# Kernel optimization log

Hardware: AMD Instinct MI355X
Metric: run time of the kernel (lower is better)

Reference implementation:

```python
import jax, jax.numpy as jnp
import numpy as np

HIDDEN = 1024
NUM_HEADS = 16
HEAD_DIM = HIDDEN // NUM_HEADS
MASK_BIAS = -10000.0


def setup_inputs() -> dict:
    key = jax.random.key(0)
    ks = jax.random.split(key, 5)
    B, S = 4, 2048
    hidden_states = jax.random.normal(ks[0], (B, S, HIDDEN), dtype=jnp.float32)
    # fused QKV projection (Linear1D_Col): hidden -> 3*hidden
    w_qkv = jax.random.normal(ks[1], (HIDDEN, 3 * HIDDEN), dtype=jnp.float32) * (HIDDEN ** -0.5)
    b_qkv = jax.random.normal(ks[2], (3 * HIDDEN,), dtype=jnp.float32) * 0.02
    # output dense (Linear1D_Row): hidden -> hidden
    w_dense = jax.random.normal(ks[3], (HIDDEN, HIDDEN), dtype=jnp.float32) * (HIDDEN ** -0.5)
    b_dense = jax.random.normal(ks[4], (HIDDEN,), dtype=jnp.float32) * 0.02
    return {"hidden_states": hidden_states, "w_qkv": w_qkv, "b_qkv": b_qkv,
            "w_dense": w_dense, "b_dense": b_dense}


def _split_heads(t):
    # [B, S, H*D] -> [B, H, S, D]
    B, S, _ = t.shape
    return t.reshape(B, S, NUM_HEADS, HEAD_DIM).transpose(0, 2, 1, 3)


def reference(hidden_states, w_qkv, b_qkv, w_dense, b_dense):
    B, S, _ = hidden_states.shape
    kvq = hidden_states @ w_qkv + b_qkv  # [B, S, 3*hidden]
    # NOTE: original chunk order is k, v, q (key first!)
    k, v, q = jnp.split(kvq, 3, axis=-1)
    q = _split_heads(q) * (HEAD_DIM ** -0.5)  # [B, H, S, D]
    k = _split_heads(k)
    v = _split_heads(v)
    scores = jnp.einsum('bhqd,bhkd->bhqk', q, k)  # [B, H, S, S]
    causal = jnp.tril(jnp.ones((S, S), dtype=bool))
    scores = jnp.where(causal[None, None], scores, jnp.asarray(MASK_BIAS, scores.dtype))
    dt = scores.dtype
    attn = jax.nn.softmax(scores.astype(jnp.float32), axis=-1).astype(dt)
    ctx = jnp.einsum('bhqk,bhkd->bhqd', attn, v)  # [B, H, S, D]
    ctx = ctx.transpose(0, 2, 1, 3).reshape(B, S, HIDDEN)
    return ctx @ w_dense + b_dense
```

## Files before the change

### kernel.cpp

```cpp
#include <hip/hip_runtime.h>

#define H_NUM 16
#define HD    64
#define SQ    2048
#define HID   1024
#define MTOK  8192

typedef __attribute__((ext_vector_type(8))) short bf16x8;
typedef __attribute__((ext_vector_type(4))) short s16x4;
typedef __attribute__((ext_vector_type(4))) float f32x4;

__device__ __forceinline__ short f2bf(float f) {
  union { float f; unsigned u; } v; v.f = f;
  unsigned r = v.u + 0x7fffu + ((v.u >> 16) & 1u);
  return (short)(r >> 16);
}

__device__ __forceinline__ float fexp2(float x) {
#if __has_builtin(__builtin_amdgcn_exp2f)
  return __builtin_amdgcn_exp2f(x);
#else
  return exp2f(x);
#endif
}

__device__ __forceinline__ void gload_lds16(const short* g, short* l) {
  __builtin_amdgcn_global_load_lds(
      (const __attribute__((address_space(1))) void*)g,
      (__attribute__((address_space(3))) void*)l, 16, 0, 0);
}

__global__ void k_cvt(const float* __restrict__ in, short* __restrict__ out, int n4) {
  int i = blockIdx.x * blockDim.x + threadIdx.x;
  if (i < n4) {
    float4 f = ((const float4*)in)[i];
    s16x4 o = { f2bf(f.x), f2bf(f.y), f2bf(f.z), f2bf(f.w) };
    ((s16x4*)out)[i] = o;
  }
}

__global__ void k_tr(const float* __restrict__ in, short* __restrict__ out, int R, int C) {
  __shared__ float t[32][33];
  int c0 = blockIdx.x * 32, r0 = blockIdx.y * 32;
  int tx = threadIdx.x, ty = threadIdx.y;
#pragma unroll
  for (int i = 0; i < 4; i++)
    t[ty + 8 * i][tx] = in[(size_t)(r0 + ty + 8 * i) * C + c0 + tx];
  __syncthreads();
#pragma unroll
  for (int i = 0; i < 4; i++)
    out[(size_t)(c0 + ty + 8 * i) * R + r0 + tx] = f2bf(t[tx][ty + 8 * i]);
}

template <int EPI>
__global__ __launch_bounds__(512, 2) void k_gemm(
    const short* __restrict__ A, const short* __restrict__ Bt,
    const float* __restrict__ bias,
    short* __restrict__ qbuf, short* __restrict__ kbuf, short* __restrict__ vtbuf,
    float* __restrict__ outf, int Kd) {
  __shared__ short as[2][16384];
  __shared__ short bs[2][8192];
  const int tid = threadIdx.x;
  const int w = tid >> 6, l = tid & 63;
  const int lr = l & 15, lk = l >> 4;
  const int wm = w >> 1, wn = w & 1;
  const int nwg = gridDim.x * gridDim.y;
  const int lin = blockIdx.y * gridDim.x + blockIdx.x;
  const int swz = (lin & 7) * (nwg >> 3) + (lin >> 3);
  const int m0 = (swz / gridDim.x) * 256, n0 = (swz % gridDim.x) * 128;

  const int NT = Kd >> 6;

#define STAGE_TILE(kt_, bufn_)                                            \
  do {                                                                    \
    _Pragma("unroll")                                                     \
    for (int rnd = 0; rnd < 4; ++rnd) {                                   \
      int g = rnd * 512 + tid;                                            \
      int row = g >> 3;                                                   \
      int sc_ = ((g & 7) * 8) ^ ((row & 7) * 8);                          \
      gload_lds16(A + (size_t)(m0 + row) * Kd + (kt_) + sc_,              \
                  &as[bufn_][0] + g * 8);                                 \
    }                                                                     \
    _Pragma("unroll")                                                     \
    for (int rnd = 0; rnd < 2; ++rnd) {                                   \
      int g = rnd * 512 + tid;                                            \
      int row = g >> 3;                                                   \
      int sc_ = ((g & 7) * 8) ^ ((row & 7) * 8);                          \
      gload_lds16(Bt + (size_t)(n0 + row) * Kd + (kt_) + sc_,             \
                  &bs[bufn_][0] + g * 8);                                 \
    }                                                                     \
  } while (0)

  f32x4 acc[4][4] = {};

  STAGE_TILE(0, 0);

  int buf = 0;
  for (int t = 0; t < NT; ++t) {
    if (t + 1 < NT) {
      STAGE_TILE((t + 1) * 64, buf ^ 1);
      asm volatile("s_waitcnt vmcnt(6)" ::: "memory");
    } else {
      asm volatile("s_waitcnt vmcnt(0)" ::: "memory");
    }
    __builtin_amdgcn_s_barrier();
    __builtin_amdgcn_sched_barrier(0);

    const short* ab = &as[buf][0];
    const short* bb = &bs[buf][0];
    const int cswz = (lr & 7) * 8;
    bf16x8 af[2][4], bfr[2][2];
#pragma unroll
    for (int kk = 0; kk < 2; ++kk)
#pragma unroll
      for (int m = 0; m < 4; ++m) {
        int row = wm * 64 + m * 16 + lr;
        af[kk][m] = *(const bf16x8*)(ab + row * 64 + ((kk * 32 + lk * 8) ^ cswz));
      }
#pragma unroll
    for (int ph = 0; ph < 2; ++ph) {
#pragma unroll
      for (int kk = 0; kk < 2; ++kk)
#pragma unroll
        for (int n = 0; n < 2; ++n) {
          int row = wn * 64 + (ph * 2 + n) * 16 + lr;
          bfr[kk][n] = *(const bf16x8*)(bb + row * 64 + ((kk * 32 + lk * 8) ^ cswz));
        }
      __builtin_amdgcn_s_setprio(1);
#pragma unroll
      for (int kk = 0; kk < 2; ++kk)
#pragma unroll
        for (int m = 0; m < 4; ++m)
#pragma unroll
          for (int n = 0; n < 2; ++n)
            acc[m][ph * 2 + n] = __builtin_amdgcn_mfma_f32_16x16x32_bf16(
                af[kk][m], bfr[kk][n], acc[m][ph * 2 + n], 0, 0, 0);
      __builtin_amdgcn_s_setprio(0);
    }
    __builtin_amdgcn_sched_barrier(0);
    __builtin_amdgcn_s_barrier();
    buf ^= 1;
  }
#undef STAGE_TILE

  const float SCLQ = 0.125f * 1.44269504088896341f;
#pragma unroll
  for (int n = 0; n < 4; ++n) {
    const int col = n0 + wn * 64 + n * 16 + lr;
    const float bv = bias[col];
    if (EPI == 1) {
#pragma unroll
      for (int m = 0; m < 4; ++m) {
        int row = m0 + wm * 64 + m * 16 + lk * 4;
#pragma unroll
        for (int r = 0; r < 4; ++r)
          outf[(size_t)(row + r) * HID + col] = acc[m][n][r] + bv;
      }
    } else if (col < HID) {
      int h = col >> 6, d = col & 63;
#pragma unroll
      for (int m = 0; m < 4; ++m) {
        int row = m0 + wm * 64 + m * 16 + lk * 4;
        int b = row >> 11, s = row & 2047;
#pragma unroll
        for (int r = 0; r < 4; ++r)
          kbuf[((size_t)(b * H_NUM + h) * SQ + s + r) * HD + d] = f2bf(acc[m][n][r] + bv);
      }
    } else if (col < 2 * HID) {
      int f = col - HID, h = f >> 6, d = f & 63;
#pragma unroll
      for (int m = 0; m < 4; ++m) {
        int row = m0 + wm * 64 + m * 16 + lk * 4;
        int b = row >> 11, s = row & 2047;
        s16x4 pk;
#pragma unroll
        for (int r = 0; r < 4; ++r) pk[r] = f2bf(acc[m][n][r] + bv);
        *(s16x4*)&vtbuf[((size_t)(b * H_NUM + h) * HD + d) * SQ + s] = pk;
      }
    } else {
      int f = col - 2 * HID, h = f >> 6, d = f & 63;
#pragma unroll
      for (int m = 0; m < 4; ++m) {
        int row = m0 + wm * 64 + m * 16 + lk * 4;
        int b = row >> 11, s = row & 2047;
#pragma unroll
        for (int r = 0; r < 4; ++r)
          qbuf[((size_t)(b * H_NUM + h) * SQ + s + r) * HD + d] = f2bf((acc[m][n][r] + bv) * SCLQ);
      }
    }
  }
}

__global__ __launch_bounds__(512) void k_attn(
    const short* __restrict__ Q, const short* __restrict__ K,
    const short* __restrict__ Vt, short* __restrict__ ctx) {
  __shared__ short ks[2][4096];
  __shared__ short vs[2][4096];
  __shared__ short ps[8][16][72];
  const int tid = threadIdx.x;
  const int w = tid >> 6, l = tid & 63;
  const int lr = l & 15, lk = l >> 4;
  const int bh = blockIdx.y;
  const int bb = bh >> 4, hh = bh & 15;
  const size_t base = (size_t)bh * (SQ * HD);
  const float THR = 11.5416f;

  const int srow = tid >> 3;
  const int scol = ((tid & 7) * 8) ^ ((srow & 7) * 8);
  const short* kg0 = K + base + srow * HD + scol;
  const short* vg0 = Vt + base + (size_t)srow * SQ + scol;
  short* kld = &ks[0][0] + tid * 8;
  short* vld = &vs[0][0] + tid * 8;
  const int rdswz = (lr & 7) * 8;

  int buf = 0;
  for (int pass = 0; pass < 2; ++pass) {
    const int qt = pass ? (15 - blockIdx.x) : blockIdx.x;
    const int nt = 2 * qt + 2;
    const int diag = 2 * qt + (w >> 2);
    const int qr = qt * 128 + w * 16;

    bf16x8 qf[2];
#pragma unroll
    for (int kk = 0; kk < 2; ++kk)
      qf[kk] = *(const bf16x8*)(Q + base + (size_t)(qr + lr) * HD + kk * 32 + lk * 8);

    f32x4 o[4] = {};
    float mrun = -3.0e4f, lsum = 0.f;

    gload_lds16(kg0, kld + buf * 4096);
    gload_lds16(vg0, vld + buf * 4096);
    __syncthreads();

    for (int t = 0; t < nt; ++t) {
      if (t + 1 < nt) {
        gload_lds16(kg0 + (t + 1) * 4096, kld + (buf ^ 1) * 4096);
        gload_lds16(vg0 + (t + 1) * 64, vld + (buf ^ 1) * 4096);
      }
      if (t <= diag) {
        const short* kb = &ks[buf][0];
        const short* vb = &vs[buf][0];
        f32x4 sf[4] = {};
        __builtin_amdgcn_s_setprio(1);
#pragma unroll
        for (int kk = 0; kk < 2; ++kk)
#pragma unroll
          for (int n = 0; n < 4; ++n) {
            bf16x8 kf = *(const bf16x8*)(kb + (n * 16 + lr) * 64 + ((kk * 32 + lk * 8) ^ rdswz));
            sf[n] = __builtin_amdgcn_mfma_f32_16x16x32_bf16(kf, qf[kk], sf[n], 0, 0, 0);
          }
        __builtin_amdgcn_s_setprio(0);

        if (t == diag) {
          const int qg = qr + lr;
#pragma unroll
          for (int n = 0; n < 4; ++n) {
            int kg = t * 64 + n * 16 + lk * 4;
#pragma unroll
            for (int r = 0; r < 4; ++r)
              if (kg + r > qg) sf[n][r] = -14426.95f;
          }
        }

        float m0 = sf[0][0];
#pragma unroll
        for (int n = 0; n < 4; ++n)
#pragma unroll
          for (int r = 0; r < 4; ++r) m0 = fmaxf(m0, sf[n][r]);
        m0 = fmaxf(m0, __shfl_xor(m0, 16));
        m0 = fmaxf(m0, __shfl_xor(m0, 32));

        if (__any(m0 > mrun + THR)) {
          float mn = fmaxf(mrun, m0);
          float sc = fexp2(mrun - mn);
          float scq[4];
#pragma unroll
          for (int r = 0; r < 4; ++r) scq[r] = __shfl(sc, lk * 4 + r);
#pragma unroll
          for (int nd = 0; nd < 4; ++nd)
#pragma unroll
            for (int r = 0; r < 4; ++r) o[nd][r] *= scq[r];
          lsum *= sc;
          mrun = mn;
        }

        float rs = 0.f;
#pragma unroll
        for (int n = 0; n < 4; ++n) {
          s16x4 pk;
#pragma unroll
          for (int r = 0; r < 4; ++r) {
            float p = fexp2(sf[n][r] - mrun);
            rs += p;
            pk[r] = (short)(__float_as_uint(p) >> 16);
          }
          *(s16x4*)&ps[w][lr][n * 16 + lk * 4] = pk;
        }
        lsum += rs;

        bf16x8 pa[2];
#pragma unroll
        for (int kk = 0; kk < 2; ++kk)
          pa[kk] = *(const bf16x8*)&ps[w][lr][kk * 32 + lk * 8];

        __builtin_amdgcn_s_setprio(1);
#pragma unroll
        for (int kk = 0; kk < 2; ++kk)
#pragma unroll
          for (int nd = 0; nd < 4; ++nd) {
            bf16x8 vf = *(const bf16x8*)(vb + (nd * 16 + lr) * 64 + ((kk * 32 + lk * 8) ^ rdswz));
            o[nd] = __builtin_amdgcn_mfma_f32_16x16x32_bf16(pa[kk], vf, o[nd], 0, 0, 0);
          }
        __builtin_amdgcn_s_setprio(0);
      }
      __syncthreads();
      buf ^= 1;
    }

    lsum += __shfl_xor(lsum, 16);
    lsum += __shfl_xor(lsum, 32);
    float inv = 1.0f / lsum;
    float invq[4];
#pragma unroll
    for (int r = 0; r < 4; ++r) invq[r] = __shfl(inv, lk * 4 + r);
#pragma unroll
    for (int nd = 0; nd < 4; ++nd)
#pragma unroll
      for (int r = 0; r < 4; ++r) {
        int s = qr + lk * 4 + r;
        ctx[((size_t)(bb * SQ + s)) * HID + hh * 64 + nd * 16 + lr] = f2bf(o[nd][r] * invq[r]);
      }
  }
}

extern "C" void kernel_launch(void* const* d_in, const int* in_sizes, int n_in,
                              void* d_out, int out_size, void* d_ws, size_t ws_size,
                              hipStream_t stream) {
  const float* hs   = (const float*)d_in[0];
  const float* wqkv = (const float*)d_in[1];
  const float* bqkv = (const float*)d_in[2];
  const float* wd   = (const float*)d_in[3];
  const float* bd   = (const float*)d_in[4];
  float* out = (float*)d_out;
  char* ws = (char*)d_ws;
  const size_t MB = 1u << 20;

  short* hs_bf  = (short*)(ws);
  short* wqkv_t = (short*)(ws + 16 * MB);
  short* wd_t   = (short*)(ws + 22 * MB);
  short* qbuf   = (short*)(ws + 24 * MB);
  short* kbuf   = (short*)(ws + 40 * MB);
  short* vtbuf  = (short*)(ws + 56 * MB);
  short* ctx    = (short*)(ws + 72 * MB);

  k_cvt<<<8192, 256, 0, stream>>>(hs, hs_bf, MTOK * HID / 4);
  k_tr<<<dim3(96, 32), dim3(32, 8), 0, stream>>>(wqkv, wqkv_t, 1024, 3072);
  k_tr<<<dim3(32, 32), dim3(32, 8), 0, stream>>>(wd, wd_t, 1024, 1024);
  k_gemm<0><<<dim3(24, 32), 512, 0, stream>>>(hs_bf, wqkv_t, bqkv,
                                              qbuf, kbuf, vtbuf, nullptr, 1024);
  k_attn<<<dim3(8, 64), 512, 0, stream>>>(qbuf, kbuf, vtbuf, ctx);
  k_gemm<1><<<dim3(8, 32), 512, 0, stream>>>(ctx, wd_t, bd,
                                             nullptr, nullptr, nullptr, out, 1024);
}
```

Before: 177.4 us.

## Triple-buffer GEMM LDS tiles and interleave global loads with MFMA phases

Moves the projection GEMM from double to triple LDS buffering, prefetching two K-tiles ahead. The global-to-LDS loads are split across four sub-phases of each K-step and interleaved with LDS fragment reads and MFMA groups, separated by barriers. The aim is to hide global memory latency and spread issue pressure. In exchange LDS use rises from 96KB to 144KB per block, which may break the two-blocks-per-CU launch bound, and the extra barriers per iteration add synchronisation overhead.

```diff
diff --git a/kernel.cpp b/kernel.cpp
--- a/kernel.cpp
+++ b/kernel.cpp
@@ -58,8 +58,8 @@
     const float* __restrict__ bias,
     short* __restrict__ qbuf, short* __restrict__ kbuf, short* __restrict__ vtbuf,
     float* __restrict__ outf, int Kd) {
-  __shared__ short as[2][16384];
-  __shared__ short bs[2][8192];
+  __shared__ short as[3][16384];
+  __shared__ short bs[3][8192];
   const int tid = threadIdx.x;
   const int w = tid >> 6, l = tid & 63;
   const int lr = l & 15, lk = l >> 4;
@@ -71,77 +71,81 @@
 
   const int NT = Kd >> 6;
 
-#define STAGE_TILE(kt_, bufn_)                                            \
-  do {                                                                    \
-    _Pragma("unroll")                                                     \
-    for (int rnd = 0; rnd < 4; ++rnd) {                                   \
-      int g = rnd * 512 + tid;                                            \
-      int row = g >> 3;                                                   \
-      int sc_ = ((g & 7) * 8) ^ ((row & 7) * 8);                          \
-      gload_lds16(A + (size_t)(m0 + row) * Kd + (kt_) + sc_,              \
-                  &as[bufn_][0] + g * 8);                                 \
-    }                                                                     \
-    _Pragma("unroll")                                                     \
-    for (int rnd = 0; rnd < 2; ++rnd) {                                   \
-      int g = rnd * 512 + tid;                                            \
-      int row = g >> 3;                                                   \
-      int sc_ = ((g & 7) * 8) ^ ((row & 7) * 8);                          \
-      gload_lds16(Bt + (size_t)(n0 + row) * Kd + (kt_) + sc_,             \
-                  &bs[bufn_][0] + g * 8);                                 \
-    }                                                                     \
-  } while (0)
+#define STAGE_A(kt_, bufn_, rnd_)                                         \
+  {                                                                       \
+    int g = (rnd_) * 512 + tid;                                           \
+    int row = g >> 3;                                                     \
+    int sc_ = ((g & 7) * 8) ^ ((row & 7) * 8);                            \
+    gload_lds16(A + (size_t)(m0 + row) * Kd + (kt_) + sc_,                \
+                &as[bufn_][0] + g * 8);                                   \
+  }
+#define STAGE_B(kt_, bufn_, rnd_)                                         \
+  {                                                                       \
+    int g = (rnd_) * 512 + tid;                                           \
+    int row = g >> 3;                                                     \
+    int sc_ = ((g & 7) * 8) ^ ((row & 7) * 8);                            \
+    gload_lds16(Bt + (size_t)(n0 + row) * Kd + (kt_) + sc_,               \
+                &bs[bufn_][0] + g * 8);                                   \
+  }
 
   f32x4 acc[4][4] = {};
-
-  STAGE_TILE(0, 0);
-
-  int buf = 0;
+  const int cswz = (lr & 7) * 8;
+
+  STAGE_A(0, 0, 0) STAGE_A(0, 0, 1) STAGE_A(0, 0, 2) STAGE_A(0, 0, 3)
+  STAGE_B(0, 0, 0) STAGE_B(0, 0, 1)
+  STAGE_A(64, 1, 0) STAGE_A(64, 1, 1) STAGE_A(64, 1, 2) STAGE_A(64, 1, 3)
+  STAGE_B(64, 1, 0) STAGE_B(64, 1, 1)
+  asm volatile("s_waitcnt vmcnt(6)" ::: "memory");
+  __builtin_amdgcn_s_barrier();
+
+  int bufR = 0;
   for (int t = 0; t < NT; ++t) {
-    if (t + 1 < NT) {
-      STAGE_TILE((t + 1) * 64, buf ^ 1);
-      asm volatile("s_waitcnt vmcnt(6)" ::: "memory");
-    } else {
-      asm volatile("s_waitcnt vmcnt(0)" ::: "memory");
+    const short* ab = &as[bufR][0];
+    const short* bb = &bs[bufR][0];
+    int bufS = bufR + 2; if (bufS >= 3) bufS -= 3;
+    const bool st = (t + 2 < NT);
+    const int ktn = (t + 2) * 64;
+
+    bf16x8 af[4], bfr[2];
+#pragma unroll
+    for (int p = 0; p < 4; ++p) {
+      const int kk = p >> 1, nh = p & 1;
+      if (nh == 0) {
+#pragma unroll
+        for (int m = 0; m < 4; ++m)
+          af[m] = *(const bf16x8*)(ab + (wm * 64 + m * 16 + lr) * 64 +
+                                   ((kk * 32 + lk * 8) ^ cswz));
+      }
+#pragma unroll
+      for (int n = 0; n < 2; ++n)
+        bfr[n] = *(const bf16x8*)(bb + (wn * 64 + (nh * 2 + n) * 16 + lr) * 64 +
+                                  ((kk * 32 + lk * 8) ^ cswz));
+      if (st) {
+        if (p == 0) { STAGE_A(ktn, bufS, 0) STAGE_A(ktn, bufS, 1) }
+        if (p == 1) { STAGE_A(ktn, bufS, 2) STAGE_A(ktn, bufS, 3) }
+        if (p == 2) { STAGE_B(ktn, bufS, 0) STAGE_B(ktn, bufS, 1) }
+      }
+      if (p == 3) {
+        if (t < NT - 2) asm volatile("s_waitcnt vmcnt(6)" ::: "memory");
+        else            asm volatile("s_waitcnt vmcnt(0)" ::: "memory");
+      }
+      __builtin_amdgcn_s_barrier();
+      asm volatile("s_waitcnt lgkmcnt(0)" ::: "memory");
+      __builtin_amdgcn_sched_barrier(0);
+      __builtin_amdgcn_s_setprio(1);
+#pragma unroll
+      for (int m = 0; m < 4; ++m)
+#pragma unroll
+        for (int n = 0; n < 2; ++n)
+          acc[m][nh * 2 + n] = __builtin_amdgcn_mfma_f32_16x16x32_bf16(
+              af[m], bfr[n], acc[m][nh * 2 + n], 0, 0, 0);
+      __builtin_amdgcn_s_setprio(0);
+      __builtin_amdgcn_s_barrier();
     }
-    __builtin_amdgcn_s_barrier();
-    __builtin_amdgcn_sched_barrier(0);
-
-    const short* ab = &as[buf][0];
-    const short* bb = &bs[buf][0];
-    const int cswz = (lr & 7) * 8;
-    bf16x8 af[2][4], bfr[2][2];
-#pragma unroll
-    for (int kk = 0; kk < 2; ++kk)
-#pragma unroll
-      for (int m = 0; m < 4; ++m) {
-        int row = wm * 64 + m * 16 + lr;
-        af[kk][m] = *(const bf16x8*)(ab + row * 64 + ((kk * 32 + lk * 8) ^ cswz));
-      }
-#pragma unroll
-    for (int ph = 0; ph < 2; ++ph) {
-#pragma unroll
-      for (int kk = 0; kk < 2; ++kk)
-#pragma unroll
-        for (int n = 0; n < 2; ++n) {
-          int row = wn * 64 + (ph * 2 + n) * 16 + lr;
-          bfr[kk][n] = *(const bf16x8*)(bb + row * 64 + ((kk * 32 + lk * 8) ^ cswz));
-        }
-      __builtin_amdgcn_s_setprio(1);
-#pragma unroll
-      for (int kk = 0; kk < 2; ++kk)
-#pragma unroll
-        for (int m = 0; m < 4; ++m)
-#pragma unroll
-          for (int n = 0; n < 2; ++n)
-            acc[m][ph * 2 + n] = __builtin_amdgcn_mfma_f32_16x16x32_bf16(
-                af[kk][m], bfr[kk][n], acc[m][ph * 2 + n], 0, 0, 0);
-      __builtin_amdgcn_s_setprio(0);
-    }
-    __builtin_amdgcn_sched_barrier(0);
-    __builtin_amdgcn_s_barrier();
-    buf ^= 1;
-  }
-#undef STAGE_TILE
+    bufR = (bufR == 2) ? 0 : bufR + 1;
+  }
+#undef STAGE_A
+#undef STAGE_B
 
   const float SCLQ = 0.125f * 1.44269504088896341f;
 #pragma unroll
```

New measurement: 185.1 us. 1.04x slower.
